# Kernel optimization log

Measured on AMD Instinct MI355X. Metric: run time of the kernel, lower is better.

Reference implementation:

```python
import jax, jax.numpy as jnp
import numpy as np

B, N, C = 2, 50000, 81          # images, proposals/image, classes (incl. background)
H, W = 800.0, 1333.0            # image shape
SCORE_THRESH = 0.05
NMS_THRESH = 0.5
DETS = 100                      # detections_per_img
K = 2048                        # pre-NMS candidates kept per image (padded)
BBOX_CLIP = 4.135166556742356   # log(1000/16), torchvision BoxCoder clamp
WX, WY, WW, WH = 10.0, 10.0, 5.0, 5.0  # bbox_reg_weights
MIN_SIZE = 0.01                 # remove_small_boxes threshold
LBL_OFFSET = 1401.0             # MAX_SIZE + 1, batched_nms class-offset trick


def setup_inputs() -> dict:
    key = jax.random.key(0)
    k1, k2, k3, k4 = jax.random.split(key, 4)
    class_logits = jax.random.normal(k1, (B * N, C), jnp.float32) * 2.0
    box_regression = jax.random.normal(k2, (B * N, C * 4), jnp.float32) * 0.5
    wh_img = jnp.array([W, H], jnp.float32)
    cxy = jax.random.uniform(k3, (B, N, 2), jnp.float32) * wh_img
    wh = jax.random.uniform(k4, (B, N, 2), jnp.float32) * 200.0 + 4.0
    x1y1 = jnp.clip(cxy - 0.5 * wh, 0.0, wh_img)
    x2y2 = jnp.clip(cxy + 0.5 * wh, 0.0, wh_img)
    proposals = jnp.concatenate([x1y1, x2y2], axis=-1)  # [B, N, 4] xyxy
    return {"class_logits": class_logits, "box_regression": box_regression, "proposals": proposals}


def _decode(rel, boxes):
    # rel [N, C, 4], boxes [N, 4] xyxy -> decoded [N, C, 4] (torchvision BoxCoder.decode)
    w = boxes[:, 2] - boxes[:, 0]
    h = boxes[:, 3] - boxes[:, 1]
    cx = boxes[:, 0] + 0.5 * w
    cy = boxes[:, 1] + 0.5 * h
    dx = rel[..., 0] / WX
    dy = rel[..., 1] / WY
    dw = jnp.minimum(rel[..., 2] / WW, BBOX_CLIP)
    dh = jnp.minimum(rel[..., 3] / WH, BBOX_CLIP)
    pcx = dx * w[:, None] + cx[:, None]
    pcy = dy * h[:, None] + cy[:, None]
    pw = jnp.exp(dw) * w[:, None]
    ph = jnp.exp(dh) * h[:, None]
    return jnp.stack([pcx - 0.5 * pw, pcy - 0.5 * ph, pcx + 0.5 * pw, pcy + 0.5 * ph], axis=-1)


def _pairwise_iou(a):
    # a [K, 4] -> [K, K]
    area = (a[:, 2] - a[:, 0]) * (a[:, 3] - a[:, 1])
    lt = jnp.maximum(a[:, None, :2], a[None, :, :2])
    rb = jnp.minimum(a[:, None, 2:], a[None, :, 2:])
    wh = jnp.clip(rb - lt, 0.0)
    inter = wh[..., 0] * wh[..., 1]
    return inter / (area[:, None] + area[None, :] - inter + 1e-9)


def _nms_keep(iou, valid):
    # sequential greedy NMS over score-sorted candidates
    Kn = iou.shape[0]
    def body(keep, i):
        sup = jnp.any(keep & (iou[i] > NMS_THRESH))
        keep = keep.at[i].set(valid[i] & ~sup)
        return keep, None
    keep, _ = jax.lax.scan(body, jnp.zeros((Kn,), bool), jnp.arange(Kn))
    return keep


def _per_image(logits, reg, props):
    # logits [N, C], reg [N, C*4], props [N, 4]
    scores = jax.nn.softmax(logits, axis=-1)[:, 1:]                  # drop background
    boxes = _decode(reg.reshape(N, C, 4), props)[:, 1:]              # [N, C-1, 4]
    boxes = jnp.stack([jnp.clip(boxes[..., 0], 0.0, W),
                       jnp.clip(boxes[..., 1], 0.0, H),
                       jnp.clip(boxes[..., 2], 0.0, W),
                       jnp.clip(boxes[..., 3], 0.0, H)], axis=-1)
    fb = boxes.reshape(-1, 4)                                        # [N*(C-1), 4]
    fs = scores.reshape(-1)
    fl = jnp.broadcast_to(jnp.arange(1, C), (N, C - 1)).reshape(-1)
    ws = fb[:, 2] - fb[:, 0]
    hs = fb[:, 3] - fb[:, 1]
    valid = (fs > SCORE_THRESH) & (ws >= MIN_SIZE) & (hs >= MIN_SIZE)
    masked = jnp.where(valid, fs, -1.0)
    top_s, top_i = jax.lax.top_k(masked, K)                          # sorted desc
    cb = fb[top_i]
    cl = fl[top_i]
    cvalid = top_s > 0.0
    # batched NMS: offset boxes by class so different classes never overlap
    ob = cb + cl.astype(cb.dtype)[:, None] * LBL_OFFSET
    keep = _nms_keep(_pairwise_iou(ob), cvalid)
    kept_s = jnp.where(keep, top_s, -1.0)
    out_s, sel = jax.lax.top_k(kept_s, DETS)
    m = out_s > 0.0
    out_b = cb[sel] * m[:, None].astype(cb.dtype)
    out_l = jnp.where(m, cl[sel], -1)
    return out_b, jnp.where(m, out_s, 0.0), out_l


def reference(class_logits, box_regression, proposals):
    logits = class_logits.reshape(B, N, C)
    reg = box_regression.reshape(B, N, C * 4)
    boxes, scores, labels = jax.vmap(_per_image)(logits, reg, proposals)
    return boxes, scores, labels  # [B, DETS, 4], [B, DETS], [B, DETS] (padded, score==0 invalid)
```

## Files before the change

kernel.cpp:

```cpp
#include <hip/hip_runtime.h>
#include <hip/hip_bf16.h>
#include <stdint.h>

#define Bn 2
#define Np 50000
#define Cc 81
#define CM1 80
#define KSEL 2048
#define NDET 100
#define NBUCK 2048
#define BUCK_BASE 0x3D000000u
#define BUCK_SHIFT 15
#define SELCAP 4096
#define IMG_W 1333.0f
#define IMG_H 800.0f
#define SCORE_TH 0.05f
#define MIN_SZ 0.01f
#define NMS_TH 0.5f
#define LBLOFF 1401.0f
#define BBOX_CLIP_F 4.135166556742356f
#define CHUNK 32
#define QCAP 320
#define BLKX 391
#define WPI  (BLKX*4)
#define RS_WPB 4

typedef unsigned long long u64;
typedef unsigned int u32;

__device__ __forceinline__ u64 shfl64(u64 v, int src) {
  int lo = __shfl((int)(u32)v, src, 64);
  int hi = __shfl((int)(u32)(v >> 32), src, 64);
  return ((u64)(u32)hi << 32) | (u32)lo;
}

__device__ __forceinline__ void decode_box(int row, int c,
    const float* __restrict__ reg, const float* __restrict__ props,
    float& x1, float& y1, float& x2, float& y2) {
  const float4 pr = *reinterpret_cast<const float4*>(props + (size_t)row * 4);
  float w = __fsub_rn(pr.z, pr.x), h = __fsub_rn(pr.w, pr.y);
  float cx = __fadd_rn(pr.x, 0.5f * w), cy = __fadd_rn(pr.y, 0.5f * h);
  const float4 rel = *reinterpret_cast<const float4*>(reg + ((size_t)row * Cc + c) * 4);
  float dx = __fdiv_rn(rel.x, 10.f), dy = __fdiv_rn(rel.y, 10.f);
  float dw = fminf(__fdiv_rn(rel.z, 5.f), BBOX_CLIP_F);
  float dh = fminf(__fdiv_rn(rel.w, 5.f), BBOX_CLIP_F);
  float pcx = __fadd_rn(__fmul_rn(dx, w), cx);
  float pcy = __fadd_rn(__fmul_rn(dy, h), cy);
  float pw = __fmul_rn(expf(dw), w);
  float ph = __fmul_rn(expf(dh), h);
  x1 = fminf(fmaxf(__fsub_rn(pcx, 0.5f * pw), 0.f), IMG_W);
  y1 = fminf(fmaxf(__fsub_rn(pcy, 0.5f * ph), 0.f), IMG_H);
  x2 = fminf(fmaxf(__fadd_rn(pcx, 0.5f * pw), 0.f), IMG_W);
  y2 = fminf(fmaxf(__fadd_rn(pcy, 0.5f * ph), 0.f), IMG_H);
}

__device__ __forceinline__ u32 drain(const u64* Qb, u32 n, int lane, int b,
    const float* __restrict__ reg, const float* __restrict__ props,
    u32* hist, u64* seg, u32 wout) {
  for (u32 qb = 0; qb < n; qb += 64) {
    const bool act = (qb + (u32)lane) < n;
    u64 key = act ? Qb[qb + lane] : 0ull;
    bool valid = false;
    u32 sb = 0;
    if (act) {
      sb = (u32)(key >> 32);
      const u32 idx = ~(u32)key;
      const int pn = (int)(idx / CM1);
      const int c = (int)(idx - (u32)pn * CM1) + 1;
      float x1, y1, x2, y2;
      decode_box(b * Np + pn, c, reg, props, x1, y1, x2, y2);
      valid = (__fsub_rn(x2, x1) >= MIN_SZ) && (__fsub_rn(y2, y1) >= MIN_SZ);
    }
    const u64 bal = __ballot(valid);
    if (valid) {
      seg[wout + (u32)__popcll(bal & ((1ull << lane) - 1ull))] = key;
      u32 bk = (sb - BUCK_BASE) >> BUCK_SHIFT;
      if (bk > (u32)(NBUCK - 1)) bk = NBUCK - 1;
      atomicAdd(&hist[bk], 1u);
    }
    wout += (u32)__popcll(bal);
  }
  return wout;
}

__global__ __launch_bounds__(256, 4) void passA_kernel(
    const float* __restrict__ logits, const float* __restrict__ reg,
    const float* __restrict__ props, u64* __restrict__ wseg,
    u32* __restrict__ wcnt, u32* __restrict__ ghist)
{
  __shared__ u64 qbuf[4][QCAP];
  __shared__ u32 hist[NBUCK];
  const int b = blockIdx.y;
  const int tid = threadIdx.x;
  const int wave = tid >> 6, lane = tid & 63;
  for (int i = tid; i < NBUCK; i += 256) hist[i] = 0;
  __syncthreads();

  const int wslot = (blockIdx.x << 2) + wave;
  u64* Q = qbuf[wave];
  u64* seg = wseg + (size_t)(b * WPI + wslot) * QCAP;
  u32 wout = 0;
  const int p = lane >> 2, qd = lane & 3;
  const int cnt_k = (qd == 3) ? 18 : 21;
  #pragma unroll
  for (int r = 0; r < 2; ++r) {
    const int n0 = wslot * CHUNK + r * 16;
    if (n0 >= Np) break;
    const int n_ = n0 + p;
    const float* lrow = logits + ((size_t)b * Np + n_) * Cc + qd * 21;
    float ev[21];
    #pragma unroll
    for (int k = 0; k < 21; ++k)
      ev[k] = (k < cnt_k) ? lrow[k] : -3.4e38f;
    float m = ev[0];
    #pragma unroll
    for (int k = 1; k < 21; ++k) m = fmaxf(m, ev[k]);
    m = fmaxf(m, __shfl_xor(m, 1, 64));
    m = fmaxf(m, __shfl_xor(m, 2, 64));
    float s = 0.f;
    #pragma unroll
    for (int k = 0; k < 21; ++k) {
      ev[k] = (k < cnt_k) ? expf(ev[k] - m) : 0.f;
      s += ev[k];
    }
    s += __shfl_xor(s, 1, 64);
    s += __shfl_xor(s, 2, 64);
    const float thr = SCORE_TH * s;
    u32 emask = 0;
    #pragma unroll
    for (int k = 0; k < 21; ++k) {
      const int c = qd * 21 + k;
      if (c > 0 && ev[k] > thr) emask |= (1u << k);
    }
    const u32 mycnt = __popc(emask);
    u32 inc = mycnt;
    #pragma unroll
    for (int o = 1; o < 64; o <<= 1) {
      const u32 v = (u32)__shfl_up((int)inc, o, 64);
      if (lane >= o) inc += v;
    }
    u32 pos = inc - mycnt;
    const u32 qtot = (u32)__shfl((int)inc, 63, 64);
    u32 em = emask;
    while (em) {
      const int k = (int)__builtin_ctz(em);
      em &= em - 1;
      const int c = qd * 21 + k;
      const u32 sb = __float_as_uint(__fdiv_rn(ev[k], s));
      const u32 idx = (u32)(n_ * CM1 + (c - 1));
      Q[pos++] = ((u64)sb << 32) | (u32)(~idx);
    }
    wout = drain(Q, qtot, lane, b, reg, props, hist, seg, wout);
  }
  if (lane == 0) wcnt[b * WPI + wslot] = wout;
  __syncthreads();
  for (int i = tid; i < NBUCK; i += 256) {
    const u32 v = hist[i];
    if (v) atomicAdd(&ghist[b * NBUCK + i], v);
  }
}

__global__ void thresh_kernel(const u32* __restrict__ ghist, u32* __restrict__ gT,
                              u32* __restrict__ gTot, u32* __restrict__ boffs,
                              u32* __restrict__ bfill) {
  const int b = blockIdx.x;
  const int lane = threadIdx.x;
  const u32* h = ghist + b * NBUCK;
  u32* bo = boffs + b * NBUCK;
  const int SEG = NBUCK / 64;
  u32 segsum = 0;
  for (int t = 0; t < SEG; ++t) segsum += h[lane * SEG + t];
  u32 suf = segsum;
  #pragma unroll
  for (int o = 1; o < 64; o <<= 1) {
    const u32 v = (u32)__shfl_down((int)suf, o, 64);
    if (lane + o < 64) suf += v;
  }
  u32 acc = suf - segsum;
  int myT = -1; u32 totv = 0;
  for (int t = SEG - 1; t >= 0; --t) {
    const int bk = lane * SEG + t;
    bo[bk] = acc;
    bfill[b * NBUCK + bk] = 0u;
    acc += h[bk];
    if (myT < 0 && acc >= (u32)KSEL) { myT = bk; totv = acc; }
  }
  int Tg = myT;
  #pragma unroll
  for (int o = 32; o; o >>= 1) Tg = max(Tg, __shfl_xor(Tg, o, 64));
  if (Tg < 0) {
    if (lane == 0) { gT[b] = 0u; gTot[b] = (acc < (u32)SELCAP) ? acc : (u32)SELCAP; }
  } else if (myT == Tg) {
    gT[b] = (u32)Tg;
    gTot[b] = (totv < (u32)SELCAP) ? totv : (u32)SELCAP;
  }
}

__global__ __launch_bounds__(256) void scatter_kernel(
    const u64* __restrict__ wseg, const u32* __restrict__ wcnt,
    const u32* __restrict__ gT, const u32* __restrict__ boffs,
    u32* __restrict__ bfill, u64* __restrict__ skeys)
{
  const int b = blockIdx.y;
  const u32 T = gT[b];
  const int wave = threadIdx.x >> 6, lane = threadIdx.x & 63;
  const u32 sgi = blockIdx.x * 4 + wave;
  if (sgi >= (u32)WPI) return;
  const u32 cnt = wcnt[b * WPI + sgi];
  const u64* seg = wseg + (size_t)(b * WPI + sgi) * QCAP;
  for (u32 i = lane; i < cnt; i += 64) {
    const u64 key = seg[i];
    const u32 sb = (u32)(key >> 32);
    u32 bk = (sb - BUCK_BASE) >> BUCK_SHIFT;
    if (bk > (u32)(NBUCK - 1)) bk = NBUCK - 1;
    if (bk >= T) {
      const u32 pos = boffs[b * NBUCK + bk] + atomicAdd(&bfill[b * NBUCK + bk], 1u);
      if (pos < (u32)SELCAP) skeys[(size_t)b * SELCAP + pos] = key;
    }
  }
}

__global__ __launch_bounds__(256) void runsort_kernel(
    const u64* __restrict__ skeys, u64* __restrict__ skeys2,
    const u32* __restrict__ gT, const u32* __restrict__ gTot,
    const u32* __restrict__ boffs, const u32* __restrict__ bfill)
{
  const int b = blockIdx.y;
  const int wave = threadIdx.x >> 6, lane = threadIdx.x & 63;
  const u32 bk = blockIdx.x * RS_WPB + wave;
  if (bk >= (u32)NBUCK || bk < gT[b]) return;
  const u32 total = gTot[b];
  const u32 start = boffs[b * NBUCK + bk];
  u32 L = bfill[b * NBUCK + bk];
  if (L == 0 || start >= (u32)KSEL || start >= total) return;
  if (start + L > total) L = total - start;
  const u64* run = skeys + (size_t)b * SELCAP + start;
  u64* dst = skeys2 + (size_t)b * SELCAP + start;
  if (L <= 128u) {
    const u64 k0 = (lane < (int)L) ? run[lane] : 0ull;
    const u64 k1 = (64 + lane < (int)L) ? run[64 + lane] : 0ull;
    u32 r0 = 0, r1 = 0;
    #pragma unroll
    for (int l = 0; l < 64; ++l) {
      const u64 o0 = shfl64(k0, l);
      const u64 o1 = shfl64(k1, l);
      r0 += (o0 > k0) + (o1 > k0);
      r1 += (o0 > k1) + (o1 > k1);
    }
    if (lane < (int)L) dst[r0] = k0;
    if (64 + lane < (int)L) dst[r1] = k1;
  } else {
    for (u32 i = lane; i < L; i += 64) {
      const u64 k = run[i];
      u32 r = 0;
      for (u32 q = 0; q < L; ++q) r += (run[q] > k);
      dst[r] = k;
    }
  }
}

__global__ __launch_bounds__(1024) void tail_kernel(
    const u64* __restrict__ skeys2, const u32* __restrict__ gTot,
    const float* __restrict__ reg, const float* __restrict__ props,
    float* __restrict__ out)
{
  __shared__ u64 keys[KSEL];
  __shared__ float obx1[KSEL], oby1[KSEL], obx2[KSEL], oby2[KSEL];
  __shared__ float oar[KSEL], osc[KSEL];
  __shared__ unsigned short keptIdx[NDET];
  __shared__ u32 supflags[64];
  __shared__ u32 sh_kc;
  const int b = blockIdx.x;
  const int tid = threadIdx.x;
  const int wave = tid >> 6, lane = tid & 63;
  const u32 total = gTot[b];
  if (tid == 0) sh_kc = 0;

  for (int i = tid; i < KSEL; i += 1024)
    keys[i] = (i < (int)total) ? skeys2[(size_t)b * SELCAP + i] : 0ull;
  __syncthreads();

  for (int t = tid; t < KSEL; t += 1024) {
    const u64 key = keys[t];
    float x1 = 0, y1 = 0, x2 = 0, y2 = 0, score = 0, lab = 0;
    if (key) {
      const u32 sb = (u32)(key >> 32);
      const u32 idx = ~(u32)key;
      const int n_ = (int)(idx / CM1);
      const int c = (int)(idx % CM1) + 1;
      score = __uint_as_float(sb);
      decode_box(b * Np + n_, c, reg, props, x1, y1, x2, y2);
      lab = (float)c;
    }
    const float offv = __fmul_rn(lab, LBLOFF);
    const float ox1 = __fadd_rn(x1, offv), oy1 = __fadd_rn(y1, offv);
    const float ox2 = __fadd_rn(x2, offv), oy2 = __fadd_rn(y2, offv);
    obx1[t] = ox1; oby1[t] = oy1; obx2[t] = ox2; oby2[t] = oy2;
    oar[t] = __fmul_rn(__fsub_rn(ox2, ox1), __fsub_rn(oy2, oy1));
    osc[t] = score;
  }
  __syncthreads();

  int kc = 0;
  for (int c = 0; c < 32 && kc < NDET; ++c) {
    if (tid < 64) supflags[tid] = 0;
    __syncthreads();
    const int j = (c << 6) + lane;
    const float cx1 = obx1[j], cy1 = oby1[j], cx2 = obx2[j], cy2 = oby2[j], ca = oar[j];
    bool sup = false;
    for (int k = wave; k < kc; k += 16) {
      const int ki = keptIdx[k];
      const float ltx = fmaxf(cx1, obx1[ki]), lty = fmaxf(cy1, oby1[ki]);
      const float rbx = fminf(cx2, obx2[ki]), rby = fminf(cy2, oby2[ki]);
      const float wx = fmaxf(__fsub_rn(rbx, ltx), 0.f);
      const float wy = fmaxf(__fsub_rn(rby, lty), 0.f);
      const float inter = __fmul_rn(wx, wy);
      const float denom = __fadd_rn(__fsub_rn(__fadd_rn(ca, oar[ki]), inter), 1e-9f);
      if (__fdiv_rn(inter, denom) > NMS_TH) sup = true;
    }
    if (sup) supflags[lane] = 1u;
    __syncthreads();
    if (wave == 0) {
      u64 rem = __ballot(supflags[lane] != 0u);
      u64 todo = __ballot(osc[j] > 0.f) & ~rem;
      int kcl = kc;
      while (todo && kcl < NDET) {
        const int jb = (int)__builtin_ctzll(todo);
        const int cj = (c << 6) + jb;
        if (lane == 0) keptIdx[kcl] = (unsigned short)cj;
        ++kcl;
        const float kx1 = obx1[cj], ky1 = oby1[cj], kx2 = obx2[cj], ky2 = oby2[cj], ka = oar[cj];
        const float ltx = fmaxf(kx1, cx1), lty = fmaxf(ky1, cy1);
        const float rbx = fminf(kx2, cx2), rby = fminf(ky2, cy2);
        const float wx = fmaxf(__fsub_rn(rbx, ltx), 0.f);
        const float wy = fmaxf(__fsub_rn(rby, lty), 0.f);
        const float inter = __fmul_rn(wx, wy);
        const float denom = __fadd_rn(__fsub_rn(__fadd_rn(ka, ca), inter), 1e-9f);
        const u64 w = __ballot(__fdiv_rn(inter, denom) > NMS_TH);
        rem |= w;
        todo &= ~rem;
        todo &= ~(1ull << jb);
      }
      if (lane == 0) sh_kc = (u32)kcl;
    }
    __syncthreads();
    kc = (int)sh_kc;
  }

  __syncthreads();
  const int kcl = (kc < NDET) ? kc : NDET;
  if (tid < NDET) {
    float bx1 = 0, by1 = 0, bx2 = 0, by2 = 0, sc = 0, lb = -1.f;
    if (tid < kcl) {
      const int i = keptIdx[tid];
      const u64 key = keys[i];
      const u32 idx = ~(u32)key;
      const int n_ = (int)(idx / CM1);
      const int cc = (int)(idx % CM1) + 1;
      decode_box(b * Np + n_, cc, reg, props, bx1, by1, bx2, by2);
      sc = osc[i];
      lb = (float)cc;
    }
    float* ob = out + (size_t)b * NDET * 4;
    ob[tid * 4 + 0] = bx1; ob[tid * 4 + 1] = by1;
    ob[tid * 4 + 2] = bx2; ob[tid * 4 + 3] = by2;
    out[Bn * NDET * 4 + b * NDET + tid] = sc;
    out[Bn * NDET * 4 + Bn * NDET + b * NDET + tid] = lb;
  }
}

extern "C" void kernel_launch(void* const* d_in, const int* in_sizes, int n_in,
                              void* d_out, int out_size, void* d_ws, size_t ws_size,
                              hipStream_t stream) {
  const float* logits = (const float*)d_in[0];
  const float* reg    = (const float*)d_in[1];
  const float* props  = (const float*)d_in[2];
  float* out = (float*)d_out;
  char* ws = (char*)d_ws;

  u32* gT   = (u32*)ws;
  u32* gTot = (u32*)(ws + 16);
  size_t off = 64;
  u32* ghist  = (u32*)(ws + off); off += (size_t)Bn * NBUCK * 4;
  const size_t memset_bytes = off;
  u32* bfill  = (u32*)(ws + off); off += (size_t)Bn * NBUCK * 4;
  u32* boffs  = (u32*)(ws + off); off += (size_t)Bn * NBUCK * 4;
  u64* skeys  = (u64*)(ws + off); off += (size_t)Bn * SELCAP * 8;
  u64* skeys2 = (u64*)(ws + off); off += (size_t)Bn * SELCAP * 8;
  u32* wcnt   = (u32*)(ws + off); off += (size_t)Bn * WPI * 4;
  off = (off + 255) & ~(size_t)255;
  u64* wseg   = (u64*)(ws + off); off += (size_t)Bn * WPI * QCAP * 8;
  (void)ws_size;

  hipMemsetAsync(d_ws, 0, memset_bytes, stream);
  passA_kernel<<<dim3(BLKX, Bn), 256, 0, stream>>>(logits, reg, props, wseg, wcnt, ghist);
  thresh_kernel<<<dim3(Bn), 64, 0, stream>>>(ghist, gT, gTot, boffs, bfill);
  scatter_kernel<<<dim3((WPI + 3) / 4, Bn), 256, 0, stream>>>(wseg, wcnt, gT, boffs, bfill, skeys);
  runsort_kernel<<<dim3(NBUCK / RS_WPB, Bn), 256, 0, stream>>>(skeys, skeys2, gT, gTot, boffs, bfill);
  tail_kernel<<<dim3(Bn), 1024, 0, stream>>>(skeys2, gTot, reg, props, out);
}
```

Before: 78.13 us.

## Stream NMS tail in double-buffered windows with overlapped decode

The tail kernel used to decode all 2048 candidates into shared memory before running NMS. It now decodes 256-candidate windows. Three waves prefetch and decode the next window while wave 0 runs greedy NMS on the current one against a compact list of kept boxes, and it stops early once 100 are kept. Kept boxes are stored directly, which removes the final re-decode. In exchange the block shrinks to 256 threads, and the NMS sweep is serialized on a single wave.

```diff
diff --git a/kernel.cpp b/kernel.cpp
--- a/kernel.cpp
+++ b/kernel.cpp
@@ -24,6 +24,7 @@
 #define BLKX 391
 #define WPI  (BLKX*4)
 #define RS_WPB 4
+#define WIN 256
 
 typedef unsigned long long u64;
 typedef unsigned int u32;
@@ -259,87 +260,115 @@
   }
 }
 
-__global__ __launch_bounds__(1024) void tail_kernel(
+__global__ __launch_bounds__(256) void tail_kernel(
     const u64* __restrict__ skeys2, const u32* __restrict__ gTot,
     const float* __restrict__ reg, const float* __restrict__ props,
     float* __restrict__ out)
 {
-  __shared__ u64 keys[KSEL];
-  __shared__ float obx1[KSEL], oby1[KSEL], obx2[KSEL], oby2[KSEL];
-  __shared__ float oar[KSEL], osc[KSEL];
-  __shared__ unsigned short keptIdx[NDET];
-  __shared__ u32 supflags[64];
+  __shared__ float bfx1[2][WIN], bfy1[2][WIN], bfx2[2][WIN], bfy2[2][WIN];
+  __shared__ float bfsc[2][WIN], bflb[2][WIN];
+  __shared__ float kox1[NDET], koy1[NDET], kox2[NDET], koy2[NDET], kar[NDET];
+  __shared__ float kx1[NDET], ky1[NDET], kx2[NDET], ky2[NDET], ksc[NDET], klb[NDET];
   __shared__ u32 sh_kc;
   const int b = blockIdx.x;
   const int tid = threadIdx.x;
   const int wave = tid >> 6, lane = tid & 63;
-  const u32 total = gTot[b];
+  const u32 totalg = gTot[b];
+  const u32 total = (totalg < (u32)KSEL) ? totalg : (u32)KSEL;
   if (tid == 0) sh_kc = 0;
 
-  for (int i = tid; i < KSEL; i += 1024)
-    keys[i] = (i < (int)total) ? skeys2[(size_t)b * SELCAP + i] : 0ull;
+  {
+    const u32 pos = (u32)tid;
+    float x1 = 0, y1 = 0, x2 = 0, y2 = 0, sc = 0, lb = 0;
+    if (pos < total) {
+      const u64 key = skeys2[(size_t)b * SELCAP + pos];
+      if (key) {
+        const u32 sb = (u32)(key >> 32);
+        const u32 idx = ~(u32)key;
+        const int n_ = (int)(idx / CM1);
+        const int c = (int)(idx % CM1) + 1;
+        sc = __uint_as_float(sb);
+        decode_box(b * Np + n_, c, reg, props, x1, y1, x2, y2);
+        lb = (float)c;
+      }
+    }
+    bfx1[0][tid] = x1; bfy1[0][tid] = y1; bfx2[0][tid] = x2; bfy2[0][tid] = y2;
+    bfsc[0][tid] = sc; bflb[0][tid] = lb;
+  }
   __syncthreads();
 
-  for (int t = tid; t < KSEL; t += 1024) {
-    const u64 key = keys[t];
-    float x1 = 0, y1 = 0, x2 = 0, y2 = 0, score = 0, lab = 0;
-    if (key) {
-      const u32 sb = (u32)(key >> 32);
-      const u32 idx = ~(u32)key;
-      const int n_ = (int)(idx / CM1);
-      const int c = (int)(idx % CM1) + 1;
-      score = __uint_as_float(sb);
-      decode_box(b * Np + n_, c, reg, props, x1, y1, x2, y2);
-      lab = (float)c;
-    }
-    const float offv = __fmul_rn(lab, LBLOFF);
-    const float ox1 = __fadd_rn(x1, offv), oy1 = __fadd_rn(y1, offv);
-    const float ox2 = __fadd_rn(x2, offv), oy2 = __fadd_rn(y2, offv);
-    obx1[t] = ox1; oby1[t] = oy1; obx2[t] = ox2; oby2[t] = oy2;
-    oar[t] = __fmul_rn(__fsub_rn(ox2, ox1), __fsub_rn(oy2, oy1));
-    osc[t] = score;
-  }
-  __syncthreads();
-
+  const u32 nwin = (total + WIN - 1) / WIN;
   int kc = 0;
-  for (int c = 0; c < 32 && kc < NDET; ++c) {
-    if (tid < 64) supflags[tid] = 0;
-    __syncthreads();
-    const int j = (c << 6) + lane;
-    const float cx1 = obx1[j], cy1 = oby1[j], cx2 = obx2[j], cy2 = oby2[j], ca = oar[j];
-    bool sup = false;
-    for (int k = wave; k < kc; k += 16) {
-      const int ki = keptIdx[k];
-      const float ltx = fmaxf(cx1, obx1[ki]), lty = fmaxf(cy1, oby1[ki]);
-      const float rbx = fminf(cx2, obx2[ki]), rby = fminf(cy2, oby2[ki]);
-      const float wx = fmaxf(__fsub_rn(rbx, ltx), 0.f);
-      const float wy = fmaxf(__fsub_rn(rby, lty), 0.f);
-      const float inter = __fmul_rn(wx, wy);
-      const float denom = __fadd_rn(__fsub_rn(__fadd_rn(ca, oar[ki]), inter), 1e-9f);
-      if (__fdiv_rn(inter, denom) > NMS_TH) sup = true;
-    }
-    if (sup) supflags[lane] = 1u;
-    __syncthreads();
-    if (wave == 0) {
-      u64 rem = __ballot(supflags[lane] != 0u);
-      u64 todo = __ballot(osc[j] > 0.f) & ~rem;
+  for (u32 w = 0; w < nwin && kc < NDET; ++w) {
+    const u32 cur = w & 1, nxt = cur ^ 1;
+    if (wave > 0) {
+      const u32 wb = (w + 1) * WIN;
+      for (u32 e = (u32)(tid - 64); e < (u32)WIN; e += 192) {
+        const u32 pos = wb + e;
+        float x1 = 0, y1 = 0, x2 = 0, y2 = 0, sc = 0, lb = 0;
+        if (pos < total) {
+          const u64 key = skeys2[(size_t)b * SELCAP + pos];
+          if (key) {
+            const u32 sb = (u32)(key >> 32);
+            const u32 idx = ~(u32)key;
+            const int n_ = (int)(idx / CM1);
+            const int c = (int)(idx % CM1) + 1;
+            sc = __uint_as_float(sb);
+            decode_box(b * Np + n_, c, reg, props, x1, y1, x2, y2);
+            lb = (float)c;
+          }
+        }
+        bfx1[nxt][e] = x1; bfy1[nxt][e] = y1; bfx2[nxt][e] = x2; bfy2[nxt][e] = y2;
+        bfsc[nxt][e] = sc; bflb[nxt][e] = lb;
+      }
+    } else {
       int kcl = kc;
-      while (todo && kcl < NDET) {
-        const int jb = (int)__builtin_ctzll(todo);
-        const int cj = (c << 6) + jb;
-        if (lane == 0) keptIdx[kcl] = (unsigned short)cj;
-        ++kcl;
-        const float kx1 = obx1[cj], ky1 = oby1[cj], kx2 = obx2[cj], ky2 = oby2[cj], ka = oar[cj];
-        const float ltx = fmaxf(kx1, cx1), lty = fmaxf(ky1, cy1);
-        const float rbx = fminf(kx2, cx2), rby = fminf(ky2, cy2);
-        const float wx = fmaxf(__fsub_rn(rbx, ltx), 0.f);
-        const float wy = fmaxf(__fsub_rn(rby, lty), 0.f);
-        const float inter = __fmul_rn(wx, wy);
-        const float denom = __fadd_rn(__fsub_rn(__fadd_rn(ka, ca), inter), 1e-9f);
-        const u64 w = __ballot(__fdiv_rn(inter, denom) > NMS_TH);
-        rem |= w;
-        todo &= ~rem;
-        todo &= ~(1ull << jb);
+      const u32 wb = w * WIN;
+      for (u32 base = 0; base < (u32)WIN && kcl < NDET; base += 64) {
+        const u32 pos = wb + base + lane;
+        const bool inb = pos < total;
+        const u32 e = base + lane;
+        const float x1 = bfx1[cur][e], y1 = bfy1[cur][e];
+        const float x2 = bfx2[cur][e], y2 = bfy2[cur][e];
+        const float sc = bfsc[cur][e], lb = bflb[cur][e];
+        const float offv = __fmul_rn(lb, LBLOFF);
+        const float ox1 = __fadd_rn(x1, offv), oy1 = __fadd_rn(y1, offv);
+        const float ox2 = __fadd_rn(x2, offv), oy2 = __fadd_rn(y2, offv);
+        const float ar = __fmul_rn(__fsub_rn(ox2, ox1), __fsub_rn(oy2, oy1));
+        const bool valid = inb && (sc > 0.f);
+        bool sup = false;
+        for (int k = 0; k < kcl; ++k) {
+          const float ltx = fmaxf(ox1, kox1[k]), lty = fmaxf(oy1, koy1[k]);
+          const float rbx = fminf(ox2, kox2[k]), rby = fminf(oy2, koy2[k]);
+          const float wx = fmaxf(__fsub_rn(rbx, ltx), 0.f);
+          const float wy = fmaxf(__fsub_rn(rby, lty), 0.f);
+          const float inter = __fmul_rn(wx, wy);
+          const float denom = __fadd_rn(__fsub_rn(__fadd_rn(ar, kar[k]), inter), 1e-9f);
+          if (__fdiv_rn(inter, denom) > NMS_TH) sup = true;
+        }
+        u64 rem = __ballot(sup) | ~__ballot(valid);
+        u64 todo = ~rem;
+        while (todo && kcl < NDET) {
+          const int jb = (int)__builtin_ctzll(todo);
+          const float bx1 = __shfl(ox1, jb, 64), by1 = __shfl(oy1, jb, 64);
+          const float bx2 = __shfl(ox2, jb, 64), by2 = __shfl(oy2, jb, 64);
+          const float ba  = __shfl(ar, jb, 64);
+          if (lane == jb) {
+            kox1[kcl] = ox1; koy1[kcl] = oy1; kox2[kcl] = ox2; koy2[kcl] = oy2; kar[kcl] = ar;
+            kx1[kcl] = x1; ky1[kcl] = y1; kx2[kcl] = x2; ky2[kcl] = y2; ksc[kcl] = sc; klb[kcl] = lb;
+          }
+          const float ltx = fmaxf(ox1, bx1), lty = fmaxf(oy1, by1);
+          const float rbx = fminf(ox2, bx2), rby = fminf(oy2, by2);
+          const float wx = fmaxf(__fsub_rn(rbx, ltx), 0.f);
+          const float wy = fmaxf(__fsub_rn(rby, lty), 0.f);
+          const float inter = __fmul_rn(wx, wy);
+          const float denom = __fadd_rn(__fsub_rn(__fadd_rn(ar, ba), inter), 1e-9f);
+          const u64 wsup = __ballot(__fdiv_rn(inter, denom) > NMS_TH);
+          rem |= wsup;
+          todo &= ~rem;
+          todo &= ~(1ull << jb);
+          ++kcl;
+        }
       }
       if (lane == 0) sh_kc = (u32)kcl;
     }
@@ -347,25 +376,18 @@
     kc = (int)sh_kc;
   }
 
-  __syncthreads();
   const int kcl = (kc < NDET) ? kc : NDET;
-  if (tid < NDET) {
+  for (int k = tid; k < NDET; k += 256) {
     float bx1 = 0, by1 = 0, bx2 = 0, by2 = 0, sc = 0, lb = -1.f;
-    if (tid < kcl) {
-      const int i = keptIdx[tid];
-      const u64 key = keys[i];
-      const u32 idx = ~(u32)key;
-      const int n_ = (int)(idx / CM1);
-      const int cc = (int)(idx % CM1) + 1;
-      decode_box(b * Np + n_, cc, reg, props, bx1, by1, bx2, by2);
-      sc = osc[i];
-      lb = (float)cc;
+    if (k < kcl) {
+      bx1 = kx1[k]; by1 = ky1[k]; bx2 = kx2[k]; by2 = ky2[k];
+      sc = ksc[k]; lb = klb[k];
     }
     float* ob = out + (size_t)b * NDET * 4;
-    ob[tid * 4 + 0] = bx1; ob[tid * 4 + 1] = by1;
-    ob[tid * 4 + 2] = bx2; ob[tid * 4 + 3] = by2;
-    out[Bn * NDET * 4 + b * NDET + tid] = sc;
-    out[Bn * NDET * 4 + Bn * NDET + b * NDET + tid] = lb;
+    ob[k * 4 + 0] = bx1; ob[k * 4 + 1] = by1;
+    ob[k * 4 + 2] = bx2; ob[k * 4 + 3] = by2;
+    out[Bn * NDET * 4 + b * NDET + k] = sc;
+    out[Bn * NDET * 4 + Bn * NDET + b * NDET + k] = lb;
   }
 }
 
@@ -397,5 +419,5 @@
   thresh_kernel<<<dim3(Bn), 64, 0, stream>>>(ghist, gT, gTot, boffs, bfill);
   scatter_kernel<<<dim3((WPI + 3) / 4, Bn), 256, 0, stream>>>(wseg, wcnt, gT, boffs, bfill, skeys);
   runsort_kernel<<<dim3(NBUCK / RS_WPB, Bn), 256, 0, stream>>>(skeys, skeys2, gT, gTot, boffs, bfill);
-  tail_kernel<<<dim3(Bn), 1024, 0, stream>>>(skeys2, gTot, reg, props, out);
-}
+  tail_kernel<<<dim3(Bn), 256, 0, stream>>>(skeys2, gTot, reg, props, out);
+}
```

After: 82.50 us. 5.6% more time.

## Fuse threshold, scatter, run-sort and NMS tail into one persistent kernel

Applied to the files above, without the earlier changes.

Replaces four small follow-up kernels with one persistent kernel of 128 blocks that uses a global atomic barrier between phases. The goal is to remove three kernel-launch gaps and their serialization overhead. Work in each phase is spread over the blocks with strided loops, and only block 0 per image runs the NMS tail. The per-wave segment stride also grows to 640 entries. The grid-wide barrier assumes all 128 blocks of 1024 threads are co-resident, which risks deadlock if they are not.

```diff
diff --git a/kernel.cpp b/kernel.cpp
--- a/kernel.cpp
+++ b/kernel.cpp
@@ -21,9 +21,11 @@
 #define BBOX_CLIP_F 4.135166556742356f
 #define CHUNK 32
 #define QCAP 320
+#define SEGCAP 640
 #define BLKX 391
 #define WPI  (BLKX*4)
-#define RS_WPB 4
+#define GXM 64
+#define NBLK (GXM*Bn)
 
 typedef unsigned long long u64;
 typedef unsigned int u32;
@@ -32,6 +34,17 @@
   int lo = __shfl((int)(u32)v, src, 64);
   int hi = __shfl((int)(u32)(v >> 32), src, 64);
   return ((u64)(u32)hi << 32) | (u32)lo;
+}
+
+__device__ __forceinline__ void gbar(u32* bar, u32 target) {
+  __syncthreads();
+  __threadfence();
+  if (threadIdx.x == 0) {
+    atomicAdd(bar, 1u);
+    while (atomicAdd(bar, 0u) < target) __builtin_amdgcn_s_sleep(2);
+    __threadfence();
+  }
+  __syncthreads();
 }
 
 __device__ __forceinline__ void decode_box(int row, int c,
@@ -98,7 +111,7 @@
 
   const int wslot = (blockIdx.x << 2) + wave;
   u64* Q = qbuf[wave];
-  u64* seg = wseg + (size_t)(b * WPI + wslot) * QCAP;
+  u64* seg = wseg + (size_t)(b * WPI + wslot) * SEGCAP;
   u32 wout = 0;
   const int p = lane >> 2, qd = lane & 3;
   const int cnt_k = (qd == 3) ? 18 : 21;
@@ -160,109 +173,13 @@
   }
 }
 
-__global__ void thresh_kernel(const u32* __restrict__ ghist, u32* __restrict__ gT,
-                              u32* __restrict__ gTot, u32* __restrict__ boffs,
-                              u32* __restrict__ bfill) {
-  const int b = blockIdx.x;
-  const int lane = threadIdx.x;
-  const u32* h = ghist + b * NBUCK;
-  u32* bo = boffs + b * NBUCK;
-  const int SEG = NBUCK / 64;
-  u32 segsum = 0;
-  for (int t = 0; t < SEG; ++t) segsum += h[lane * SEG + t];
-  u32 suf = segsum;
-  #pragma unroll
-  for (int o = 1; o < 64; o <<= 1) {
-    const u32 v = (u32)__shfl_down((int)suf, o, 64);
-    if (lane + o < 64) suf += v;
-  }
-  u32 acc = suf - segsum;
-  int myT = -1; u32 totv = 0;
-  for (int t = SEG - 1; t >= 0; --t) {
-    const int bk = lane * SEG + t;
-    bo[bk] = acc;
-    bfill[b * NBUCK + bk] = 0u;
-    acc += h[bk];
-    if (myT < 0 && acc >= (u32)KSEL) { myT = bk; totv = acc; }
-  }
-  int Tg = myT;
-  #pragma unroll
-  for (int o = 32; o; o >>= 1) Tg = max(Tg, __shfl_xor(Tg, o, 64));
-  if (Tg < 0) {
-    if (lane == 0) { gT[b] = 0u; gTot[b] = (acc < (u32)SELCAP) ? acc : (u32)SELCAP; }
-  } else if (myT == Tg) {
-    gT[b] = (u32)Tg;
-    gTot[b] = (totv < (u32)SELCAP) ? totv : (u32)SELCAP;
-  }
-}
-
-__global__ __launch_bounds__(256) void scatter_kernel(
+__global__ __launch_bounds__(1024) void mega_kernel(
     const u64* __restrict__ wseg, const u32* __restrict__ wcnt,
-    const u32* __restrict__ gT, const u32* __restrict__ boffs,
-    u32* __restrict__ bfill, u64* __restrict__ skeys)
-{
-  const int b = blockIdx.y;
-  const u32 T = gT[b];
-  const int wave = threadIdx.x >> 6, lane = threadIdx.x & 63;
-  const u32 sgi = blockIdx.x * 4 + wave;
-  if (sgi >= (u32)WPI) return;
-  const u32 cnt = wcnt[b * WPI + sgi];
-  const u64* seg = wseg + (size_t)(b * WPI + sgi) * QCAP;
-  for (u32 i = lane; i < cnt; i += 64) {
-    const u64 key = seg[i];
-    const u32 sb = (u32)(key >> 32);
-    u32 bk = (sb - BUCK_BASE) >> BUCK_SHIFT;
-    if (bk > (u32)(NBUCK - 1)) bk = NBUCK - 1;
-    if (bk >= T) {
-      const u32 pos = boffs[b * NBUCK + bk] + atomicAdd(&bfill[b * NBUCK + bk], 1u);
-      if (pos < (u32)SELCAP) skeys[(size_t)b * SELCAP + pos] = key;
-    }
-  }
-}
-
-__global__ __launch_bounds__(256) void runsort_kernel(
-    const u64* __restrict__ skeys, u64* __restrict__ skeys2,
-    const u32* __restrict__ gT, const u32* __restrict__ gTot,
-    const u32* __restrict__ boffs, const u32* __restrict__ bfill)
-{
-  const int b = blockIdx.y;
-  const int wave = threadIdx.x >> 6, lane = threadIdx.x & 63;
-  const u32 bk = blockIdx.x * RS_WPB + wave;
-  if (bk >= (u32)NBUCK || bk < gT[b]) return;
-  const u32 total = gTot[b];
-  const u32 start = boffs[b * NBUCK + bk];
-  u32 L = bfill[b * NBUCK + bk];
-  if (L == 0 || start >= (u32)KSEL || start >= total) return;
-  if (start + L > total) L = total - start;
-  const u64* run = skeys + (size_t)b * SELCAP + start;
-  u64* dst = skeys2 + (size_t)b * SELCAP + start;
-  if (L <= 128u) {
-    const u64 k0 = (lane < (int)L) ? run[lane] : 0ull;
-    const u64 k1 = (64 + lane < (int)L) ? run[64 + lane] : 0ull;
-    u32 r0 = 0, r1 = 0;
-    #pragma unroll
-    for (int l = 0; l < 64; ++l) {
-      const u64 o0 = shfl64(k0, l);
-      const u64 o1 = shfl64(k1, l);
-      r0 += (o0 > k0) + (o1 > k0);
-      r1 += (o0 > k1) + (o1 > k1);
-    }
-    if (lane < (int)L) dst[r0] = k0;
-    if (64 + lane < (int)L) dst[r1] = k1;
-  } else {
-    for (u32 i = lane; i < L; i += 64) {
-      const u64 k = run[i];
-      u32 r = 0;
-      for (u32 q = 0; q < L; ++q) r += (run[q] > k);
-      dst[r] = k;
-    }
-  }
-}
-
-__global__ __launch_bounds__(1024) void tail_kernel(
-    const u64* __restrict__ skeys2, const u32* __restrict__ gTot,
+    const u32* __restrict__ ghist, u32* __restrict__ gT,
+    u32* __restrict__ gTot, u32* __restrict__ boffs, u32* __restrict__ bfill,
+    u64* __restrict__ skeys, u64* __restrict__ skeys2,
     const float* __restrict__ reg, const float* __restrict__ props,
-    float* __restrict__ out)
+    float* __restrict__ out, u32* __restrict__ bar)
 {
   __shared__ u64 keys[KSEL];
   __shared__ float obx1[KSEL], oby1[KSEL], obx2[KSEL], oby2[KSEL];
@@ -270,102 +187,196 @@
   __shared__ unsigned short keptIdx[NDET];
   __shared__ u32 supflags[64];
   __shared__ u32 sh_kc;
-  const int b = blockIdx.x;
+  const int b = blockIdx.y;
   const int tid = threadIdx.x;
   const int wave = tid >> 6, lane = tid & 63;
-  const u32 total = gTot[b];
-  if (tid == 0) sh_kc = 0;
-
-  for (int i = tid; i < KSEL; i += 1024)
-    keys[i] = (i < (int)total) ? skeys2[(size_t)b * SELCAP + i] : 0ull;
-  __syncthreads();
-
-  for (int t = tid; t < KSEL; t += 1024) {
-    const u64 key = keys[t];
-    float x1 = 0, y1 = 0, x2 = 0, y2 = 0, score = 0, lab = 0;
-    if (key) {
-      const u32 sb = (u32)(key >> 32);
-      const u32 idx = ~(u32)key;
-      const int n_ = (int)(idx / CM1);
-      const int c = (int)(idx % CM1) + 1;
-      score = __uint_as_float(sb);
-      decode_box(b * Np + n_, c, reg, props, x1, y1, x2, y2);
-      lab = (float)c;
-    }
-    const float offv = __fmul_rn(lab, LBLOFF);
-    const float ox1 = __fadd_rn(x1, offv), oy1 = __fadd_rn(y1, offv);
-    const float ox2 = __fadd_rn(x2, offv), oy2 = __fadd_rn(y2, offv);
-    obx1[t] = ox1; oby1[t] = oy1; obx2[t] = ox2; oby2[t] = oy2;
-    oar[t] = __fmul_rn(__fsub_rn(ox2, ox1), __fsub_rn(oy2, oy1));
-    osc[t] = score;
-  }
-  __syncthreads();
-
-  int kc = 0;
-  for (int c = 0; c < 32 && kc < NDET; ++c) {
-    if (tid < 64) supflags[tid] = 0;
+
+  if (blockIdx.x == 0 && wave == 0) {
+    const u32* h = ghist + b * NBUCK;
+    u32* bo = boffs + b * NBUCK;
+    const int SEG = NBUCK / 64;
+    u32 segsum = 0;
+    for (int t = 0; t < SEG; ++t) segsum += h[lane * SEG + t];
+    u32 suf = segsum;
+    #pragma unroll
+    for (int o = 1; o < 64; o <<= 1) {
+      const u32 v = (u32)__shfl_down((int)suf, o, 64);
+      if (lane + o < 64) suf += v;
+    }
+    u32 acc = suf - segsum;
+    int myT = -1; u32 totv = 0;
+    for (int t = SEG - 1; t >= 0; --t) {
+      const int bk = lane * SEG + t;
+      bo[bk] = acc;
+      bfill[b * NBUCK + bk] = 0u;
+      acc += h[bk];
+      if (myT < 0 && acc >= (u32)KSEL) { myT = bk; totv = acc; }
+    }
+    int Tg = myT;
+    #pragma unroll
+    for (int o = 32; o; o >>= 1) Tg = max(Tg, __shfl_xor(Tg, o, 64));
+    if (Tg < 0) {
+      if (lane == 0) { gT[b] = 0u; gTot[b] = (acc < (u32)SELCAP) ? acc : (u32)SELCAP; }
+    } else if (myT == Tg) {
+      gT[b] = (u32)Tg;
+      gTot[b] = (totv < (u32)SELCAP) ? totv : (u32)SELCAP;
+    }
+  }
+  gbar(bar, NBLK * 1);
+
+  {
+    const u32 T = gT[b];
+    for (u32 sgi = blockIdx.x * 16 + wave; sgi < (u32)WPI; sgi += GXM * 16) {
+      const u32 cnt = wcnt[b * WPI + sgi];
+      const u64* seg = wseg + (size_t)(b * WPI + sgi) * SEGCAP;
+      for (u32 i = lane; i < cnt; i += 64) {
+        const u64 key = seg[i];
+        const u32 sb = (u32)(key >> 32);
+        u32 bk = (sb - BUCK_BASE) >> BUCK_SHIFT;
+        if (bk > (u32)(NBUCK - 1)) bk = NBUCK - 1;
+        if (bk >= T) {
+          const u32 pos = boffs[b * NBUCK + bk] + atomicAdd(&bfill[b * NBUCK + bk], 1u);
+          if (pos < (u32)SELCAP) skeys[(size_t)b * SELCAP + pos] = key;
+        }
+      }
+    }
+  }
+  gbar(bar, NBLK * 2);
+
+  {
+    const u32 T = gT[b];
+    const u32 total = gTot[b];
+    for (u32 bk = blockIdx.x * 16 + wave; bk < (u32)NBUCK; bk += GXM * 16) {
+      if (bk < T) continue;
+      const u32 start = boffs[b * NBUCK + bk];
+      u32 L = bfill[b * NBUCK + bk];
+      if (L == 0 || start >= (u32)KSEL || start >= total) continue;
+      if (start + L > total) L = total - start;
+      const u64* run = skeys + (size_t)b * SELCAP + start;
+      u64* dst = skeys2 + (size_t)b * SELCAP + start;
+      if (L <= 128u) {
+        const u64 k0 = (lane < (int)L) ? run[lane] : 0ull;
+        const u64 k1 = (64 + lane < (int)L) ? run[64 + lane] : 0ull;
+        u32 r0 = 0, r1 = 0;
+        #pragma unroll
+        for (int l = 0; l < 64; ++l) {
+          const u64 o0 = shfl64(k0, l);
+          const u64 o1 = shfl64(k1, l);
+          r0 += (o0 > k0) + (o1 > k0);
+          r1 += (o0 > k1) + (o1 > k1);
+        }
+        if (lane < (int)L) dst[r0] = k0;
+        if (64 + lane < (int)L) dst[r1] = k1;
+      } else {
+        for (u32 i = lane; i < L; i += 64) {
+          const u64 k = run[i];
+          u32 r = 0;
+          for (u32 q = 0; q < L; ++q) r += (run[q] > k);
+          dst[r] = k;
+        }
+      }
+    }
+  }
+  gbar(bar, NBLK * 3);
+
+  if (blockIdx.x != 0) return;
+  {
+    const u64* sk2 = skeys2 + (size_t)b * SELCAP;
+    const u32 totalg = gTot[b];
+    const u32 total = (totalg < (u32)KSEL) ? totalg : (u32)KSEL;
+    if (tid == 0) sh_kc = 0;
+
+    for (int i = tid; i < KSEL; i += 1024)
+      keys[i] = (i < (int)total) ? sk2[i] : 0ull;
     __syncthreads();
-    const int j = (c << 6) + lane;
-    const float cx1 = obx1[j], cy1 = oby1[j], cx2 = obx2[j], cy2 = oby2[j], ca = oar[j];
-    bool sup = false;
-    for (int k = wave; k < kc; k += 16) {
-      const int ki = keptIdx[k];
-      const float ltx = fmaxf(cx1, obx1[ki]), lty = fmaxf(cy1, oby1[ki]);
-      const float rbx = fminf(cx2, obx2[ki]), rby = fminf(cy2, oby2[ki]);
-      const float wx = fmaxf(__fsub_rn(rbx, ltx), 0.f);
-      const float wy = fmaxf(__fsub_rn(rby, lty), 0.f);
-      const float inter = __fmul_rn(wx, wy);
-      const float denom = __fadd_rn(__fsub_rn(__fadd_rn(ca, oar[ki]), inter), 1e-9f);
-      if (__fdiv_rn(inter, denom) > NMS_TH) sup = true;
-    }
-    if (sup) supflags[lane] = 1u;
+
+    for (int t = tid; t < KSEL; t += 1024) {
+      const u64 key = keys[t];
+      float x1 = 0, y1 = 0, x2 = 0, y2 = 0, score = 0, lab = 0;
+      if (key) {
+        const u32 sb = (u32)(key >> 32);
+        const u32 idx = ~(u32)key;
+        const int n_ = (int)(idx / CM1);
+        const int c = (int)(idx % CM1) + 1;
+        score = __uint_as_float(sb);
+        decode_box(b * Np + n_, c, reg, props, x1, y1, x2, y2);
+        lab = (float)c;
+      }
+      const float offv = __fmul_rn(lab, LBLOFF);
+      const float ox1 = __fadd_rn(x1, offv), oy1 = __fadd_rn(y1, offv);
+      const float ox2 = __fadd_rn(x2, offv), oy2 = __fadd_rn(y2, offv);
+      obx1[t] = ox1; oby1[t] = oy1; obx2[t] = ox2; oby2[t] = oy2;
+      oar[t] = __fmul_rn(__fsub_rn(ox2, ox1), __fsub_rn(oy2, oy1));
+      osc[t] = score;
+    }
     __syncthreads();
-    if (wave == 0) {
-      u64 rem = __ballot(supflags[lane] != 0u);
-      u64 todo = __ballot(osc[j] > 0.f) & ~rem;
-      int kcl = kc;
-      while (todo && kcl < NDET) {
-        const int jb = (int)__builtin_ctzll(todo);
-        const int cj = (c << 6) + jb;
-        if (lane == 0) keptIdx[kcl] = (unsigned short)cj;
-        ++kcl;
-        const float kx1 = obx1[cj], ky1 = oby1[cj], kx2 = obx2[cj], ky2 = oby2[cj], ka = oar[cj];
-        const float ltx = fmaxf(kx1, cx1), lty = fmaxf(ky1, cy1);
-        const float rbx = fminf(kx2, cx2), rby = fminf(ky2, cy2);
+
+    int kc = 0;
+    for (int c = 0; c < 32 && kc < NDET; ++c) {
+      if (tid < 64) supflags[tid] = 0;
+      __syncthreads();
+      const int j = (c << 6) + lane;
+      const float cx1 = obx1[j], cy1 = oby1[j], cx2 = obx2[j], cy2 = oby2[j], ca = oar[j];
+      bool sup = false;
+      for (int k = wave; k < kc; k += 16) {
+        const int ki = keptIdx[k];
+        const float ltx = fmaxf(cx1, obx1[ki]), lty = fmaxf(cy1, oby1[ki]);
+        const float rbx = fminf(cx2, obx2[ki]), rby = fminf(cy2, oby2[ki]);
         const float wx = fmaxf(__fsub_rn(rbx, ltx), 0.f);
         const float wy = fmaxf(__fsub_rn(rby, lty), 0.f);
         const float inter = __fmul_rn(wx, wy);
-        const float denom = __fadd_rn(__fsub_rn(__fadd_rn(ka, ca), inter), 1e-9f);
-        const u64 w = __ballot(__fdiv_rn(inter, denom) > NMS_TH);
-        rem |= w;
-        todo &= ~rem;
-        todo &= ~(1ull << jb);
-      }
-      if (lane == 0) sh_kc = (u32)kcl;
-    }
+        const float denom = __fadd_rn(__fsub_rn(__fadd_rn(ca, oar[ki]), inter), 1e-9f);
+        if (__fdiv_rn(inter, denom) > NMS_TH) sup = true;
+      }
+      if (sup) supflags[lane] = 1u;
+      __syncthreads();
+      if (wave == 0) {
+        u64 rem = __ballot(supflags[lane] != 0u);
+        u64 todo = __ballot(osc[j] > 0.f) & ~rem;
+        int kcl = kc;
+        while (todo && kcl < NDET) {
+          const int jb = (int)__builtin_ctzll(todo);
+          const int cj = (c << 6) + jb;
+          if (lane == 0) keptIdx[kcl] = (unsigned short)cj;
+          ++kcl;
+          const float kx1 = obx1[cj], ky1 = oby1[cj], kx2 = obx2[cj], ky2 = oby2[cj], ka = oar[cj];
+          const float ltx = fmaxf(kx1, cx1), lty = fmaxf(ky1, cy1);
+          const float rbx = fminf(kx2, cx2), rby = fminf(ky2, cy2);
+          const float wx = fmaxf(__fsub_rn(rbx, ltx), 0.f);
+          const float wy = fmaxf(__fsub_rn(rby, lty), 0.f);
+          const float inter = __fmul_rn(wx, wy);
+          const float denom = __fadd_rn(__fsub_rn(__fadd_rn(ka, ca), inter), 1e-9f);
+          const u64 w = __ballot(__fdiv_rn(inter, denom) > NMS_TH);
+          rem |= w;
+          todo &= ~rem;
+          todo &= ~(1ull << jb);
+        }
+        if (lane == 0) sh_kc = (u32)kcl;
+      }
+      __syncthreads();
+      kc = (int)sh_kc;
+    }
+
     __syncthreads();
-    kc = (int)sh_kc;
-  }
-
-  __syncthreads();
-  const int kcl = (kc < NDET) ? kc : NDET;
-  if (tid < NDET) {
-    float bx1 = 0, by1 = 0, bx2 = 0, by2 = 0, sc = 0, lb = -1.f;
-    if (tid < kcl) {
-      const int i = keptIdx[tid];
-      const u64 key = keys[i];
-      const u32 idx = ~(u32)key;
-      const int n_ = (int)(idx / CM1);
-      const int cc = (int)(idx % CM1) + 1;
-      decode_box(b * Np + n_, cc, reg, props, bx1, by1, bx2, by2);
-      sc = osc[i];
-      lb = (float)cc;
-    }
-    float* ob = out + (size_t)b * NDET * 4;
-    ob[tid * 4 + 0] = bx1; ob[tid * 4 + 1] = by1;
-    ob[tid * 4 + 2] = bx2; ob[tid * 4 + 3] = by2;
-    out[Bn * NDET * 4 + b * NDET + tid] = sc;
-    out[Bn * NDET * 4 + Bn * NDET + b * NDET + tid] = lb;
+    const int kcl = (kc < NDET) ? kc : NDET;
+    if (tid < NDET) {
+      float bx1 = 0, by1 = 0, bx2 = 0, by2 = 0, sc = 0, lb = -1.f;
+      if (tid < kcl) {
+        const int i = keptIdx[tid];
+        const u64 key = keys[i];
+        const u32 idx = ~(u32)key;
+        const int n_ = (int)(idx / CM1);
+        const int cc = (int)(idx % CM1) + 1;
+        decode_box(b * Np + n_, cc, reg, props, bx1, by1, bx2, by2);
+        sc = osc[i];
+        lb = (float)cc;
+      }
+      float* ob = out + (size_t)b * NDET * 4;
+      ob[tid * 4 + 0] = bx1; ob[tid * 4 + 1] = by1;
+      ob[tid * 4 + 2] = bx2; ob[tid * 4 + 3] = by2;
+      out[Bn * NDET * 4 + b * NDET + tid] = sc;
+      out[Bn * NDET * 4 + Bn * NDET + b * NDET + tid] = lb;
+    }
   }
 }
 
@@ -380,6 +391,7 @@
 
   u32* gT   = (u32*)ws;
   u32* gTot = (u32*)(ws + 16);
+  u32* bar  = (u32*)(ws + 32);
   size_t off = 64;
   u32* ghist  = (u32*)(ws + off); off += (size_t)Bn * NBUCK * 4;
   const size_t memset_bytes = off;
@@ -389,13 +401,11 @@
   u64* skeys2 = (u64*)(ws + off); off += (size_t)Bn * SELCAP * 8;
   u32* wcnt   = (u32*)(ws + off); off += (size_t)Bn * WPI * 4;
   off = (off + 255) & ~(size_t)255;
-  u64* wseg   = (u64*)(ws + off); off += (size_t)Bn * WPI * QCAP * 8;
+  u64* wseg   = (u64*)(ws + off); off += (size_t)Bn * WPI * SEGCAP * 8;
   (void)ws_size;
 
   hipMemsetAsync(d_ws, 0, memset_bytes, stream);
   passA_kernel<<<dim3(BLKX, Bn), 256, 0, stream>>>(logits, reg, props, wseg, wcnt, ghist);
-  thresh_kernel<<<dim3(Bn), 64, 0, stream>>>(ghist, gT, gTot, boffs, bfill);
-  scatter_kernel<<<dim3((WPI + 3) / 4, Bn), 256, 0, stream>>>(wseg, wcnt, gT, boffs, bfill, skeys);
-  runsort_kernel<<<dim3(NBUCK / RS_WPB, Bn), 256, 0, stream>>>(skeys, skeys2, gT, gTot, boffs, bfill);
-  tail_kernel<<<dim3(Bn), 1024, 0, stream>>>(skeys2, gTot, reg, props, out);
-}
+  mega_kernel<<<dim3(GXM, Bn), 1024, 0, stream>>>(wseg, wcnt, ghist, gT, gTot,
+      boffs, bfill, skeys, skeys2, reg, props, out, bar);
+}
```

Measured after the change: 219.9 us. +181.4%, slower.
